# Kernel tuning notes

Hardware: AMD Instinct MI355X
Metric: run time of the kernel (lower is better)

The kernel has to match this reference:

```python
import jax, jax.numpy as jnp
import numpy as np

N = 8192
NFEAT = 512
NHID = 512
NCLASS = 8
EPS = 1e-9
ADJ_P = 0.01  # edge density


def setup_inputs() -> dict:
    key = jax.random.key(0)
    ks = jax.random.split(key, 16)
    adj = (jax.random.uniform(ks[0], (N, N)) < ADJ_P).astype(jnp.float32)
    x = jax.random.normal(ks[1], (N, NFEAT), dtype=jnp.float32)
    s_in = 1.0 / np.sqrt(NFEAT)
    s_h = 1.0 / np.sqrt(NHID)
    return {
        "adj": adj,
        "x": x,
        "gcn1_W": jax.random.normal(ks[2], (NFEAT, NHID), jnp.float32) * s_in,
        "gcn1_b": jnp.zeros((NHID,), jnp.float32),
        "Qw": jax.random.normal(ks[3], (NHID, NHID), jnp.float32) * s_h,
        "Qb": jnp.zeros((NHID,), jnp.float32),
        "Kw": jax.random.normal(ks[4], (NHID, NHID), jnp.float32) * s_h,
        "Kb": jnp.zeros((NHID,), jnp.float32),
        "Vw": jax.random.normal(ks[5], (NHID, NHID), jnp.float32) * s_h,
        "Vb": jnp.zeros((NHID,), jnp.float32),
        "ln_g": jnp.ones((NHID,), jnp.float32),
        "ln_b": jnp.zeros((NHID,), jnp.float32),
        "gcn2_W": jax.random.normal(ks[6], (NHID, NCLASS), jnp.float32) * s_h,
        "gcn2_b": jnp.zeros((NCLASS,), jnp.float32),
    }


def _gcn_norm(a):
    # symmetric degree normalization D^{-1/2} A D^{-1/2}, degrees = row sums
    d_inv_sqrt = jax.lax.rsqrt(a.sum(axis=1) + EPS)  # [N]
    return d_inv_sqrt[:, None] * a * d_inv_sqrt[None, :]


def _layer_norm(x, g, b):
    mu = x.mean(axis=-1, keepdims=True)
    var = x.var(axis=-1, keepdims=True)
    return (x - mu) * jax.lax.rsqrt(var + 1e-5) * g + b


def reference(adj, x, gcn1_W, gcn1_b, Qw, Qb, Kw, Kb, Vw, Vb, ln_g, ln_b, gcn2_W, gcn2_b):
    # GraphConvolution: adj @ (x W) + b, then ReLU
    h = jax.nn.relu(adj @ (x @ gcn1_W) + gcn1_b)  # [N, NHID]
    Qh = h @ Qw + Qb
    Kh = h @ Kw + Kb
    Vh = h @ Vw + Vb
    # adjacency-masked dense scores (multiplicative mask, as in original)
    A_tilde = adj * (Qh @ Kh.T)  # [N, N]
    attention = jax.nn.softmax(A_tilde, axis=1)
    X_tilde = _gcn_norm(attention) @ Vh  # [N, NHID]
    X_tilde = _layer_norm(X_tilde, ln_g, ln_b)
    z = adj @ (X_tilde @ gcn2_W) + gcn2_b  # [N, NCLASS]
    return jax.nn.softmax(z, axis=1)
```

## Files before the change

### kernel.cpp

```cpp
#include <hip/hip_runtime.h>
#include <math.h>

#define N_NODES 8192
#define NFEAT 512
#define NHID 512
#define NCLASS 8
#define RCAP 192
#define KSPLIT 1536

__device__ inline ushort f2bf(float f) {
  uint32_t u = __float_as_uint(f);
  uint32_t r = u + 0x7fffu + ((u >> 16) & 1u);
  return (ushort)(r >> 16);
}
__device__ inline float bf2f(ushort h) { return __uint_as_float(((uint32_t)h) << 16); }

__global__ __launch_bounds__(256) void build_ell(const float* __restrict__ adj,
                                                 int* __restrict__ colidx,
                                                 int* __restrict__ deg) {
  int row = blockIdx.x;
  __shared__ int cnt;
  __shared__ int cols[RCAP];
  if (threadIdx.x == 0) cnt = 0;
  __syncthreads();
  const float4* arow = (const float4*)(adj + (size_t)row * N_NODES);
  for (int i = threadIdx.x; i < N_NODES / 4; i += 256) {
    float4 v = arow[i];
    int base = i * 4;
    if (v.x > 0.5f) { int p = atomicAdd(&cnt, 1); if (p < RCAP) cols[p] = base; }
    if (v.y > 0.5f) { int p = atomicAdd(&cnt, 1); if (p < RCAP) cols[p] = base + 1; }
    if (v.z > 0.5f) { int p = atomicAdd(&cnt, 1); if (p < RCAP) cols[p] = base + 2; }
    if (v.w > 0.5f) { int p = atomicAdd(&cnt, 1); if (p < RCAP) cols[p] = base + 3; }
  }
  __syncthreads();
  int d = cnt < RCAP ? cnt : RCAP;
  if (threadIdx.x == 0) deg[row] = d;
  for (int i = threadIdx.x; i < d; i += 256) colidx[(size_t)row * RCAP + i] = cols[i];
}

__global__ void transpose512(const float* __restrict__ in, float* __restrict__ out) {
  __shared__ float tile[32][33];
  int x = blockIdx.x * 32 + threadIdx.x;
  int y0 = blockIdx.y * 32;
  for (int i = threadIdx.y; i < 32; i += 8)
    tile[i][threadIdx.x] = in[(size_t)(y0 + i) * 512 + x];
  __syncthreads();
  int xo = blockIdx.y * 32 + threadIdx.x;
  int yo0 = blockIdx.x * 32;
  for (int i = threadIdx.y; i < 32; i += 8)
    out[(size_t)(yo0 + i) * 512 + xo] = tile[threadIdx.x][i];
}

__global__ __launch_bounds__(256) void sgemm64x128(const float* __restrict__ A,
                                                   const float* __restrict__ B,
                                                   const float* __restrict__ bias,
                                                   float* __restrict__ C,
                                                   int M, int Nn, int K, int ldc) {
  __shared__ float As[16][68];
  __shared__ float Bs[16][132];
  const int tid = threadIdx.x;
  const int bm = blockIdx.y * 64, bn = blockIdx.x * 128;
  const int tx = tid & 15, ty = tid >> 4;
  const int arow = tid >> 2, acol = (tid & 3) << 2;
  const int brow = tid >> 4, bcol = (tid & 15) << 2;
  float acc[4][8];
#pragma unroll
  for (int i = 0; i < 4; ++i)
#pragma unroll
    for (int j = 0; j < 8; ++j) acc[i][j] = 0.f;
  const float* Ap = A + (size_t)(bm + arow) * K + acol;
  const float* Bp = B + (size_t)brow * Nn + bn + bcol;
  float4 av = *(const float4*)(Ap);
  float4 bv0 = *(const float4*)(Bp);
  float4 bv1 = *(const float4*)(Bp + 64);
  for (int k0 = 0; k0 < K; k0 += 16) {
    if (k0) __syncthreads();
    As[acol + 0][arow] = av.x;
    As[acol + 1][arow] = av.y;
    As[acol + 2][arow] = av.z;
    As[acol + 3][arow] = av.w;
    *(float4*)&Bs[brow][bcol] = bv0;
    *(float4*)&Bs[brow][bcol + 64] = bv1;
    __syncthreads();
    int kn = (k0 + 16 < K) ? k0 + 16 : 0;
    av = *(const float4*)(Ap + kn);
    bv0 = *(const float4*)(Bp + (size_t)kn * Nn);
    bv1 = *(const float4*)(Bp + (size_t)kn * Nn + 64);
#pragma unroll
    for (int kk = 0; kk < 16; ++kk) {
      float4 a = *(const float4*)&As[kk][ty << 2];
      float4 b0 = *(const float4*)&Bs[kk][tx << 2];
      float4 b1 = *(const float4*)&Bs[kk][(tx << 2) + 64];
      float ar[4] = {a.x, a.y, a.z, a.w};
      float br[8] = {b0.x, b0.y, b0.z, b0.w, b1.x, b1.y, b1.z, b1.w};
#pragma unroll
      for (int i = 0; i < 4; ++i)
#pragma unroll
        for (int j = 0; j < 8; ++j) acc[i][j] = fmaf(ar[i], br[j], acc[i][j]);
    }
  }
#pragma unroll
  for (int i = 0; i < 4; ++i) {
    int r = bm + (ty << 2) + i;
    float4 o0 = make_float4(acc[i][0], acc[i][1], acc[i][2], acc[i][3]);
    float4 o1 = make_float4(acc[i][4], acc[i][5], acc[i][6], acc[i][7]);
    if (bias) {
      const float4 z0 = *(const float4*)(bias + bn + (tx << 2));
      const float4 z1 = *(const float4*)(bias + bn + 64 + (tx << 2));
      o0.x += z0.x; o0.y += z0.y; o0.z += z0.z; o0.w += z0.w;
      o1.x += z1.x; o1.y += z1.y; o1.z += z1.z; o1.w += z1.w;
    }
    *(float4*)(C + (size_t)r * ldc + bn + (tx << 2)) = o0;
    *(float4*)(C + (size_t)r * ldc + bn + 64 + (tx << 2)) = o1;
  }
}

__global__ __launch_bounds__(256) void split_a(const float* __restrict__ A, ushort* __restrict__ As) {
  int idx = blockIdx.x * 256 + threadIdx.x;
  int m = idx >> 7, t = idx & 127;
  float4 v = ((const float4*)(A + (size_t)m * 512))[t];
  ushort4 hi, lo;
  hi.x = f2bf(v.x); hi.y = f2bf(v.y); hi.z = f2bf(v.z); hi.w = f2bf(v.w);
  lo.x = f2bf(v.x - bf2f(hi.x)); lo.y = f2bf(v.y - bf2f(hi.y));
  lo.z = f2bf(v.z - bf2f(hi.z)); lo.w = f2bf(v.w - bf2f(hi.w));
  ushort* row = As + (size_t)m * KSPLIT;
  ((ushort4*)row)[t] = hi;
  ((ushort4*)(row + 512))[t] = hi;
  ((ushort4*)(row + 1024))[t] = lo;
}

__global__ __launch_bounds__(256) void split_bt(const float* __restrict__ B, ushort* __restrict__ Bt, int Nn) {
  int idx = blockIdx.x * 256 + threadIdx.x;
  int n = idx / 384, t = idx % 384;
  int sec = t >> 7;
  int k0 = (t & 127) << 2;
  ushort4 o;
  float f0 = B[(size_t)(k0 + 0) * Nn + n];
  float f1 = B[(size_t)(k0 + 1) * Nn + n];
  float f2 = B[(size_t)(k0 + 2) * Nn + n];
  float f3 = B[(size_t)(k0 + 3) * Nn + n];
  if (sec == 1) {
    o.x = f2bf(f0 - bf2f(f2bf(f0))); o.y = f2bf(f1 - bf2f(f2bf(f1)));
    o.z = f2bf(f2 - bf2f(f2bf(f2))); o.w = f2bf(f3 - bf2f(f2bf(f3)));
  } else {
    o.x = f2bf(f0); o.y = f2bf(f1); o.z = f2bf(f2); o.w = f2bf(f3);
  }
  ((ushort4*)(Bt + (size_t)n * KSPLIT))[t] = o;
}

__global__ __launch_bounds__(256) void split_bt_cat(const float* __restrict__ Mm, const float* __restrict__ Vw,
                                                    ushort* __restrict__ Bt) {
  int idx = blockIdx.x * 256 + threadIdx.x;
  int n = idx / 384, t = idx % 384;
  const float* src = (n < 512) ? (Mm + n) : (Vw + (n - 512));
  int sec = t >> 7;
  int k0 = (t & 127) << 2;
  ushort4 o;
  float f0 = src[(size_t)(k0 + 0) * 512];
  float f1 = src[(size_t)(k0 + 1) * 512];
  float f2 = src[(size_t)(k0 + 2) * 512];
  float f3 = src[(size_t)(k0 + 3) * 512];
  if (sec == 1) {
    o.x = f2bf(f0 - bf2f(f2bf(f0))); o.y = f2bf(f1 - bf2f(f2bf(f1)));
    o.z = f2bf(f2 - bf2f(f2bf(f2))); o.w = f2bf(f3 - bf2f(f2bf(f3)));
  } else {
    o.x = f2bf(f0); o.y = f2bf(f1); o.z = f2bf(f2); o.w = f2bf(f3);
  }
  ((ushort4*)(Bt + (size_t)n * KSPLIT))[t] = o;
}

__global__ void build_bcat(const float* __restrict__ Vb, float* __restrict__ bcat) {
  int i = blockIdx.x * 256 + threadIdx.x;
  bcat[i] = (i < 512) ? 0.f : Vb[i - 512];
}

using frag_ab = __attribute__((ext_vector_type(8))) short;
using frag_cd = __attribute__((ext_vector_type(4))) float;

__global__ __launch_bounds__(256) void mfma_gemm_bt(const ushort* __restrict__ A,
                                                    const ushort* __restrict__ Bt,
                                                    const float* __restrict__ bias,
                                                    float* __restrict__ C,
                                                    int M, int N, int K, int ldc) {
  __shared__ __align__(16) ushort Atile[128 * 64];
  __shared__ __align__(16) ushort Btile[128 * 64];
  const int tid = threadIdx.x;
  const int w = tid >> 6, lane = tid & 63;
  const int m0 = blockIdx.y * 128, n0 = blockIdx.x * 128;
  const int wm = (w >> 1) * 64, wn = (w & 1) * 64;
  const int q = lane >> 4, c = lane & 15;

  frag_cd acc[4][4] = {{{0.f, 0.f, 0.f, 0.f}}};
#pragma unroll
  for (int i = 0; i < 4; ++i)
#pragma unroll
    for (int j = 0; j < 4; ++j) acc[i][j] = (frag_cd){0.f, 0.f, 0.f, 0.f};

  const int srow = (w << 3) + (lane >> 3);
  const int scolb = (lane & 7) << 4;
  const uint8_t* gA = (const uint8_t*)A + ((size_t)(m0 + srow) * K) * 2 + scolb;
  const uint8_t* gB = (const uint8_t*)Bt + ((size_t)(n0 + srow) * K) * 2 + scolb;
  const size_t rowpitch = (size_t)K * 2;

  for (int k0 = 0; k0 < K; k0 += 64) {
    const size_t kb = (size_t)k0 * 2;
#pragma unroll
    for (int r = 0; r < 4; ++r) {
      __builtin_amdgcn_global_load_lds(
          (const __attribute__((address_space(1))) uint32_t*)(gA + (size_t)(r * 32) * rowpitch + kb),
          (__attribute__((address_space(3))) uint32_t*)((uint8_t*)Atile + r * 4096 + w * 1024), 16, 0, 0);
      __builtin_amdgcn_global_load_lds(
          (const __attribute__((address_space(1))) uint32_t*)(gB + (size_t)(r * 32) * rowpitch + kb),
          (__attribute__((address_space(3))) uint32_t*)((uint8_t*)Btile + r * 4096 + w * 1024), 16, 0, 0);
    }
    __syncthreads();
#pragma unroll
    for (int kk = 0; kk < 2; ++kk) {
      frag_ab af[4], bf[4];
#pragma unroll
      for (int i = 0; i < 4; ++i) {
        af[i] = *(const frag_ab*)((const uint8_t*)Atile + (wm + i * 16 + c) * 128 + kk * 64 + q * 16);
        bf[i] = *(const frag_ab*)((const uint8_t*)Btile + (wn + i * 16 + c) * 128 + kk * 64 + q * 16);
      }
#pragma unroll
      for (int i = 0; i < 4; ++i)
#pragma unroll
        for (int j = 0; j < 4; ++j)
          acc[i][j] = __builtin_amdgcn_mfma_f32_16x16x32_bf16(af[i], bf[j], acc[i][j], 0, 0, 0);
    }
    __syncthreads();
  }
#pragma unroll
  for (int j = 0; j < 4; ++j) {
    int col = n0 + wn + j * 16 + c;
    float bv = bias ? bias[col] : 0.f;
#pragma unroll
    for (int i = 0; i < 4; ++i) {
      int row = m0 + wm + i * 16 + q * 4;
#pragma unroll
      for (int r = 0; r < 4; ++r)
        C[(size_t)(row + r) * ldc + col] = acc[i][j][r] + bv;
    }
  }
}

__global__ __launch_bounds__(64) void bias_prep(const float* __restrict__ Qw, const float* __restrict__ Kw,
                                                const float* __restrict__ Qb, const float* __restrict__ Kb,
                                                float* __restrict__ u, float* __restrict__ w,
                                                float* __restrict__ cbuf) {
  int k = blockIdx.x;
  int lane = threadIdx.x;
  if (k == NHID) {
    float s = 0.f;
    for (int j = lane; j < NHID; j += 64) s = fmaf(Qb[j], Kb[j], s);
#pragma unroll
    for (int o = 32; o > 0; o >>= 1) s += __shfl_down(s, o, 64);
    if (lane == 0) cbuf[0] = s;
    return;
  }
  float su = 0.f, sw = 0.f;
  for (int j = lane; j < NHID; j += 64) {
    su = fmaf(Qw[(size_t)k * NHID + j], Kb[j], su);
    sw = fmaf(Kw[(size_t)k * NHID + j], Qb[j], sw);
  }
#pragma unroll
  for (int o = 32; o > 0; o >>= 1) { su += __shfl_down(su, o, 64); sw += __shfl_down(sw, o, 64); }
  if (lane == 0) { u[k] = su; w[k] = sw; }
}

__global__ __launch_bounds__(128) void spmm_bias_relu(const float* __restrict__ xW,
                                                      const int* __restrict__ colidx,
                                                      const int* __restrict__ deg,
                                                      const float* __restrict__ bias,
                                                      float* __restrict__ h,
                                                      ushort* __restrict__ Hs) {
  int row = blockIdx.x;
  int d = deg[row];
  __shared__ int scols[RCAP];
  int t = threadIdx.x;
  for (int i = t; i < d; i += 128) scols[i] = colidx[(size_t)row * RCAP + i];
  __syncthreads();
  float4 acc = make_float4(0.f, 0.f, 0.f, 0.f);
  int e = 0;
  for (; e + 8 <= d; e += 8) {
    float4 v0 = ((const float4*)(xW + (size_t)scols[e + 0] * NHID))[t];
    float4 v1 = ((const float4*)(xW + (size_t)scols[e + 1] * NHID))[t];
    float4 v2 = ((const float4*)(xW + (size_t)scols[e + 2] * NHID))[t];
    float4 v3 = ((const float4*)(xW + (size_t)scols[e + 3] * NHID))[t];
    float4 v4 = ((const float4*)(xW + (size_t)scols[e + 4] * NHID))[t];
    float4 v5 = ((const float4*)(xW + (size_t)scols[e + 5] * NHID))[t];
    float4 v6 = ((const float4*)(xW + (size_t)scols[e + 6] * NHID))[t];
    float4 v7 = ((const float4*)(xW + (size_t)scols[e + 7] * NHID))[t];
    acc.x += ((v0.x + v1.x) + (v2.x + v3.x)) + ((v4.x + v5.x) + (v6.x + v7.x));
    acc.y += ((v0.y + v1.y) + (v2.y + v3.y)) + ((v4.y + v5.y) + (v6.y + v7.y));
    acc.z += ((v0.z + v1.z) + (v2.z + v3.z)) + ((v4.z + v5.z) + (v6.z + v7.z));
    acc.w += ((v0.w + v1.w) + (v2.w + v3.w)) + ((v4.w + v5.w) + (v6.w + v7.w));
  }
  for (; e < d; ++e) {
    float4 v = ((const float4*)(xW + (size_t)scols[e] * NHID))[t];
    acc.x += v.x; acc.y += v.y; acc.z += v.z; acc.w += v.w;
  }
  float4 bv = ((const float4*)bias)[t];
  float4 o = make_float4(fmaxf(acc.x + bv.x, 0.f), fmaxf(acc.y + bv.y, 0.f),
                         fmaxf(acc.z + bv.z, 0.f), fmaxf(acc.w + bv.w, 0.f));
  ((float4*)(h + (size_t)row * NHID))[t] = o;
  ushort4 hi, lo;
  hi.x = f2bf(o.x); hi.y = f2bf(o.y); hi.z = f2bf(o.z); hi.w = f2bf(o.w);
  lo.x = f2bf(o.x - bf2f(hi.x)); lo.y = f2bf(o.y - bf2f(hi.y));
  lo.z = f2bf(o.z - bf2f(hi.z)); lo.w = f2bf(o.w - bf2f(hi.w));
  ushort* hr = Hs + (size_t)row * KSPLIT;
  ((ushort4*)hr)[t] = hi;
  ((ushort4*)(hr + 512))[t] = hi;
  ((ushort4*)(hr + 1024))[t] = lo;
}

__global__ __launch_bounds__(256) void dual_matvec(const float* __restrict__ h, const float* __restrict__ u,
                                                   const float* __restrict__ w, float* __restrict__ a_vec,
                                                   float* __restrict__ b_vec) {
  int t = threadIdx.x;
  int wv = t >> 6, lane = t & 63;
  int row = blockIdx.x * 4 + wv;
  const float2* hr = (const float2*)(h + (size_t)row * NHID);
  const float2* ur = (const float2*)u;
  const float2* wr = (const float2*)w;
  float sa = 0.f, sb = 0.f;
  for (int i = lane; i < NHID / 2; i += 64) {
    float2 hv = hr[i], uv = ur[i], wv2 = wr[i];
    sa = fmaf(hv.x, uv.x, sa); sa = fmaf(hv.y, uv.y, sa);
    sb = fmaf(hv.x, wv2.x, sb); sb = fmaf(hv.y, wv2.y, sb);
  }
#pragma unroll
  for (int o = 32; o > 0; o >>= 1) { sa += __shfl_down(sa, o, 64); sb += __shfl_down(sb, o, 64); }
  if (lane == 0) { a_vec[row] = sa; b_vec[row] = sb; }
}

__global__ void zero_vec(float* __restrict__ T) { T[threadIdx.x] = 0.f; }

__global__ __launch_bounds__(256) void colsum_atomic(const float* __restrict__ Vh, int ldv,
                                                     float* __restrict__ T) {
  int t = threadIdx.x;
  int r0 = blockIdx.x * 128;
  float2 s = make_float2(0.f, 0.f);
  for (int r = 0; r < 128; ++r) {
    float2 v = ((const float2*)(Vh + (size_t)(r0 + r) * ldv))[t];
    s.x += v.x;
    s.y += v.y;
  }
  atomicAdd(&T[2 * t], s.x);
  atomicAdd(&T[2 * t + 1], s.y);
}

__global__ __launch_bounds__(256) void edge_softmax_agg(const float* __restrict__ G, int ldg,
                                                        const float* __restrict__ h,
                                                        const float* __restrict__ Vh, int ldv,
                                                        const int* __restrict__ colidx, const int* __restrict__ deg,
                                                        const float* __restrict__ a_vec, const float* __restrict__ b_vec,
                                                        const float* __restrict__ cbuf, const float* __restrict__ T,
                                                        const float* __restrict__ lng, const float* __restrict__ lnb,
                                                        float* __restrict__ Xt) {
  __shared__ float gs[4][NHID];
  __shared__ int scols[4][RCAP];
  __shared__ float sbv[4][RCAP];
  __shared__ float sv[4][RCAP];
  int t = threadIdx.x, wv = t >> 6, lane = t & 63;
  int row = blockIdx.x * 4 + wv;
  int d = deg[row];
  const float4* gr = (const float4*)(G + (size_t)row * ldg);
  ((float4*)gs[wv])[lane] = gr[lane];
  ((float4*)gs[wv])[64 + lane] = gr[64 + lane];
  for (int i = lane; i < d; i += 64) {
    int cc = colidx[(size_t)row * RCAP + i];
    scols[wv][i] = cc;
    sbv[wv][i] = b_vec[cc];
  }
  __syncthreads();
  float ai = a_vec[row] + cbuf[0];
  int q = lane >> 4, u = lane & 15;
  const float4* gq = (const float4*)gs[wv] + u;
  for (int e0 = 0; e0 < d; e0 += 4) {
    int e = e0 + q;
    bool act = e < d;
    int col = act ? scols[wv][e] : 0;
    const float4* hr = (const float4*)(h + (size_t)col * NHID) + u;
    float s_a = 0.f, s_b = 0.f;
#pragma unroll
    for (int it = 0; it < 8; it += 2) {
      float4 h0 = hr[it * 16], g0 = gq[it * 16];
      float4 h1 = hr[(it + 1) * 16], g1 = gq[(it + 1) * 16];
      s_a = fmaf(h0.x, g0.x, s_a); s_a = fmaf(h0.y, g0.y, s_a);
      s_a = fmaf(h0.z, g0.z, s_a); s_a = fmaf(h0.w, g0.w, s_a);
      s_b = fmaf(h1.x, g1.x, s_b); s_b = fmaf(h1.y, g1.y, s_b);
      s_b = fmaf(h1.z, g1.z, s_b); s_b = fmaf(h1.w, g1.w, s_b);
    }
    float s = s_a + s_b;
    s += __shfl_down(s, 8, 16);
    s += __shfl_down(s, 4, 16);
    s += __shfl_down(s, 2, 16);
    s += __shfl_down(s, 1, 16);
    if (u == 0 && act) sv[wv][e] = s + ai + sbv[wv][e];
  }
  __syncthreads();
  float m = 0.f;
  for (int i = lane; i < d; i += 64) m = fmaxf(m, sv[wv][i]);
#pragma unroll
  for (int o = 32; o > 0; o >>= 1) m = fmaxf(m, __shfl_xor(m, o, 64));
  float ssum = 0.f;
  for (int i = lane; i < d; i += 64) {
    float ex = expf(sv[wv][i] - m);
    sv[wv][i] = ex;
    ssum += ex;
  }
#pragma unroll
  for (int o = 32; o > 0; o >>= 1) ssum += __shfl_xor(ssum, o, 64);
  float em = expf(-m);
  float inv = 1.f / (ssum + (float)(N_NODES - d) * em);
  float ci = em * inv;
  __syncthreads();
  float4 a0 = make_float4(0.f, 0.f, 0.f, 0.f), a1 = a0;
  for (int e = 0; e < d; ++e) {
    float we = sv[wv][e] * inv;
    if (we > 1e-12f) {
      const float4* vr = (const float4*)(Vh + (size_t)scols[wv][e] * ldv);
      float4 v0 = vr[lane * 2], v1 = vr[lane * 2 + 1];
      a0.x = fmaf(we, v0.x, a0.x); a0.y = fmaf(we, v0.y, a0.y);
      a0.z = fmaf(we, v0.z, a0.z); a0.w = fmaf(we, v0.w, a0.w);
      a1.x = fmaf(we, v1.x, a1.x); a1.y = fmaf(we, v1.y, a1.y);
      a1.z = fmaf(we, v1.z, a1.z); a1.w = fmaf(we, v1.w, a1.w);
    }
  }
  float4 t0 = ((const float4*)T)[lane * 2], t1 = ((const float4*)T)[lane * 2 + 1];
  a0.x = fmaf(ci, t0.x, a0.x); a0.y = fmaf(ci, t0.y, a0.y);
  a0.z = fmaf(ci, t0.z, a0.z); a0.w = fmaf(ci, t0.w, a0.w);
  a1.x = fmaf(ci, t1.x, a1.x); a1.y = fmaf(ci, t1.y, a1.y);
  a1.z = fmaf(ci, t1.z, a1.z); a1.w = fmaf(ci, t1.w, a1.w);
  float s1 = ((a0.x + a0.y) + (a0.z + a0.w)) + ((a1.x + a1.y) + (a1.z + a1.w));
  float s2 = ((a0.x * a0.x + a0.y * a0.y) + (a0.z * a0.z + a0.w * a0.w)) +
             ((a1.x * a1.x + a1.y * a1.y) + (a1.z * a1.z + a1.w * a1.w));
#pragma unroll
  for (int o = 32; o > 0; o >>= 1) { s1 += __shfl_xor(s1, o, 64); s2 += __shfl_xor(s2, o, 64); }
  float mu = s1 * (1.f / NHID);
  float var = s2 * (1.f / NHID) - mu * mu;
  float rstd = rsqrtf(var + 1e-5f);
  float4 g0 = ((const float4*)lng)[lane * 2], g1 = ((const float4*)lng)[lane * 2 + 1];
  float4 b0 = ((const float4*)lnb)[lane * 2], b1 = ((const float4*)lnb)[lane * 2 + 1];
  float4 o0, o1;
  o0.x = (a0.x - mu) * rstd * g0.x + b0.x;
  o0.y = (a0.y - mu) * rstd * g0.y + b0.y;
  o0.z = (a0.z - mu) * rstd * g0.z + b0.z;
  o0.w = (a0.w - mu) * rstd * g0.w + b0.w;
  o1.x = (a1.x - mu) * rstd * g1.x + b1.x;
  o1.y = (a1.y - mu) * rstd * g1.y + b1.y;
  o1.z = (a1.z - mu) * rstd * g1.z + b1.z;
  o1.w = (a1.w - mu) * rstd * g1.w + b1.w;
  float4* xr = (float4*)(Xt + (size_t)row * NHID);
  xr[lane * 2] = o0;
  xr[lane * 2 + 1] = o1;
}

__global__ __launch_bounds__(256) void xt_w2(const float* __restrict__ Xt, const float* __restrict__ W2,
                                             float* __restrict__ Y) {
  __shared__ float w2s[NHID * NCLASS];
  int t = threadIdx.x;
  for (int i = t; i < NHID * NCLASS; i += 256) w2s[i] = W2[i];
  __syncthreads();
  int wv = t >> 6, lane = t & 63;
  int row = blockIdx.x * 4 + wv;
  const float4* xr = (const float4*)(Xt + (size_t)row * NHID);
  float4 x0 = xr[lane * 2], x1 = xr[lane * 2 + 1];
  float xv[8] = {x0.x, x0.y, x0.z, x0.w, x1.x, x1.y, x1.z, x1.w};
  float acc[NCLASS];
#pragma unroll
  for (int c = 0; c < NCLASS; ++c) acc[c] = 0.f;
#pragma unroll
  for (int kk = 0; kk < 8; ++kk) {
    int k = lane * 8 + kk;
#pragma unroll
    for (int c = 0; c < NCLASS; ++c) acc[c] = fmaf(xv[kk], w2s[k * NCLASS + c], acc[c]);
  }
#pragma unroll
  for (int c = 0; c < NCLASS; ++c)
#pragma unroll
    for (int o = 32; o > 0; o >>= 1) acc[c] += __shfl_down(acc[c], o, 64);
  if (lane == 0) {
    *(float4*)(Y + (size_t)row * NCLASS) = make_float4(acc[0], acc[1], acc[2], acc[3]);
    *(float4*)(Y + (size_t)row * NCLASS + 4) = make_float4(acc[4], acc[5], acc[6], acc[7]);
  }
}

__global__ __launch_bounds__(256) void final_spmm_softmax(const float* __restrict__ Y,
                                                          const int* __restrict__ colidx,
                                                          const int* __restrict__ deg,
                                                          const float* __restrict__ b2,
                                                          float* __restrict__ out) {
  int t = threadIdx.x;
  int wv = t >> 6, lane = t & 63;
  int row = blockIdx.x * 4 + wv;
  int d = deg[row];
  const int* cols = colidx + (size_t)row * RCAP;
  float acc[8];
#pragma unroll
  for (int c = 0; c < 8; ++c) acc[c] = 0.f;
  for (int e = lane; e < d; e += 64) {
    int col = cols[e];
    const float4* yr = (const float4*)(Y + (size_t)col * 8);
    float4 y0 = yr[0], y1 = yr[1];
    acc[0] += y0.x; acc[1] += y0.y; acc[2] += y0.z; acc[3] += y0.w;
    acc[4] += y1.x; acc[5] += y1.y; acc[6] += y1.z; acc[7] += y1.w;
  }
#pragma unroll
  for (int c = 0; c < 8; ++c)
#pragma unroll
    for (int o = 32; o > 0; o >>= 1) acc[c] += __shfl_down(acc[c], o, 64);
  if (lane == 0) {
    float z[8];
    float m = -1e30f;
#pragma unroll
    for (int c = 0; c < 8; ++c) { z[c] = acc[c] + b2[c]; m = fmaxf(m, z[c]); }
    float s = 0.f;
#pragma unroll
    for (int c = 0; c < 8; ++c) { z[c] = expf(z[c] - m); s += z[c]; }
    float inv = 1.f / s;
    *(float4*)(out + (size_t)row * 8) = make_float4(z[0] * inv, z[1] * inv, z[2] * inv, z[3] * inv);
    *(float4*)(out + (size_t)row * 8 + 4) = make_float4(z[4] * inv, z[5] * inv, z[6] * inv, z[7] * inv);
  }
}

extern "C" void kernel_launch(void* const* d_in, const int* in_sizes, int n_in,
                              void* d_out, int out_size, void* d_ws, size_t ws_size,
                              hipStream_t stream) {
  const float* adj = (const float*)d_in[0];
  const float* x = (const float*)d_in[1];
  const float* W1 = (const float*)d_in[2];
  const float* b1 = (const float*)d_in[3];
  const float* Qw = (const float*)d_in[4];
  const float* Qb = (const float*)d_in[5];
  const float* Kw = (const float*)d_in[6];
  const float* Kb = (const float*)d_in[7];
  const float* Vw = (const float*)d_in[8];
  const float* Vb = (const float*)d_in[9];
  const float* ln_g = (const float*)d_in[10];
  const float* ln_b = (const float*)d_in[11];
  const float* W2 = (const float*)d_in[12];
  const float* b2 = (const float*)d_in[13];
  float* out = (float*)d_out;

  char* ws = (char*)d_ws;
  size_t off = 0;
  auto alloc = [&](size_t bytes) -> void* {
    void* p = ws + off;
    off = (off + bytes + 255) & ~(size_t)255;
    return p;
  };
  int* colidx = (int*)alloc((size_t)N_NODES * RCAP * 4);
  int* deg = (int*)alloc((size_t)N_NODES * 4);
  float* bufA = (float*)alloc((size_t)N_NODES * NHID * 4);
  float* bufB = (float*)alloc((size_t)N_NODES * NHID * 4);
  float* GVh = (float*)alloc((size_t)N_NODES * 1024 * 4);
  ushort* Xs = (ushort*)alloc((size_t)N_NODES * KSPLIT * 2);
  ushort* Hs = (ushort*)alloc((size_t)N_NODES * KSPLIT * 2);
  ushort* W1ts = (ushort*)alloc((size_t)512 * KSPLIT * 2);
  ushort* Bcts = (ushort*)alloc((size_t)1024 * KSPLIT * 2);
  float* KwT = (float*)alloc((size_t)512 * 512 * 4);
  float* Mmat = (float*)alloc((size_t)512 * 512 * 4);
  float* bcat = (float*)alloc((size_t)1024 * 4);
  float* a_vec = (float*)alloc((size_t)N_NODES * 4);
  float* b_vec = (float*)alloc((size_t)N_NODES * 4);
  float* u_vec = (float*)alloc((size_t)NHID * 4);
  float* w_vec = (float*)alloc((size_t)NHID * 4);
  float* cbuf = (float*)alloc(256);
  float* T = (float*)alloc((size_t)NHID * 4);
  float* Y = (float*)alloc((size_t)N_NODES * NCLASS * 4);
  (void)in_sizes; (void)n_in; (void)out_size; (void)ws_size;

  build_ell<<<N_NODES, 256, 0, stream>>>(adj, colidx, deg);
  transpose512<<<dim3(16, 16), dim3(32, 8), 0, stream>>>(Kw, KwT);
  bias_prep<<<NHID + 1, 64, 0, stream>>>(Qw, Kw, Qb, Kb, u_vec, w_vec, cbuf);
  sgemm64x128<<<dim3(4, 8), 256, 0, stream>>>(Qw, KwT, nullptr, Mmat, 512, 512, 512, 512);
  split_a<<<(N_NODES * 128) / 256, 256, 0, stream>>>(x, Xs);
  split_bt<<<(512 * 384) / 256, 256, 0, stream>>>(W1, W1ts, 512);
  mfma_gemm_bt<<<dim3(4, 64), 256, 0, stream>>>(Xs, W1ts, nullptr, bufA, N_NODES, 512, KSPLIT, 512);
  spmm_bias_relu<<<N_NODES, 128, 0, stream>>>(bufA, colidx, deg, b1, bufB, Hs);
  split_bt_cat<<<(1024 * 384) / 256, 256, 0, stream>>>(Mmat, Vw, Bcts);
  build_bcat<<<4, 256, 0, stream>>>(Vb, bcat);
  mfma_gemm_bt<<<dim3(8, 64), 256, 0, stream>>>(Hs, Bcts, bcat, GVh, N_NODES, 1024, KSPLIT, 1024);
  dual_matvec<<<N_NODES / 4, 256, 0, stream>>>(bufB, u_vec, w_vec, a_vec, b_vec);
  zero_vec<<<1, 512, 0, stream>>>(T);
  colsum_atomic<<<64, 256, 0, stream>>>(GVh + 512, 1024, T);
  edge_softmax_agg<<<N_NODES / 4, 256, 0, stream>>>(GVh, 1024, bufB, GVh + 512, 1024, colidx, deg,
                                                    a_vec, b_vec, cbuf, T, ln_g, ln_b, bufA);
  xt_w2<<<N_NODES / 4, 256, 0, stream>>>(bufA, W2, Y);
  final_spmm_softmax<<<N_NODES / 4, 256, 0, stream>>>(Y, colidx, deg, b2, out);
}
```

Measured before the change: 850.7 us.

## Slice sparse gathers by column range and shrink split-bf16 A operand

The SpMM and the edge-score gathers are split into 8 passes, each touching only neighbour columns inside one 1024-row window. The aim is to keep each window of the gathered matrix resident in cache. The split-bf16 A operand drops its duplicated hi copy: the MFMA GEMM now reuses the first 512 columns for two of the three K-segments, which cuts A-side memory and write traffic. The bias/ReLU/bf16 split and the dual matvec are fused into one finalize kernel, and scores are staged through a global edge buffer before a separate softmax/aggregate/layernorm kernel. The cost is many more launches, repeated colidx scans, and a read-modify-write of h on every slice.

After: 812.3 us. -4.5%, faster.

```diff
diff --git a/kernel.cpp b/kernel.cpp
--- a/kernel.cpp
+++ b/kernel.cpp
@@ -6,7 +6,9 @@
 #define NHID 512
 #define NCLASS 8
 #define RCAP 192
-#define KSPLIT 1536
+#define KB_SPLIT 1536
+#define KA_SPLIT 1024
+#define NSLICE 8
 
 __device__ inline ushort f2bf(float f) {
   uint32_t u = __float_as_uint(f);
@@ -53,7 +55,6 @@
 
 __global__ __launch_bounds__(256) void sgemm64x128(const float* __restrict__ A,
                                                    const float* __restrict__ B,
-                                                   const float* __restrict__ bias,
                                                    float* __restrict__ C,
                                                    int M, int Nn, int K, int ldc) {
   __shared__ float As[16][68];
@@ -102,20 +103,14 @@
 #pragma unroll
   for (int i = 0; i < 4; ++i) {
     int r = bm + (ty << 2) + i;
-    float4 o0 = make_float4(acc[i][0], acc[i][1], acc[i][2], acc[i][3]);
-    float4 o1 = make_float4(acc[i][4], acc[i][5], acc[i][6], acc[i][7]);
-    if (bias) {
-      const float4 z0 = *(const float4*)(bias + bn + (tx << 2));
-      const float4 z1 = *(const float4*)(bias + bn + 64 + (tx << 2));
-      o0.x += z0.x; o0.y += z0.y; o0.z += z0.z; o0.w += z0.w;
-      o1.x += z1.x; o1.y += z1.y; o1.z += z1.z; o1.w += z1.w;
-    }
-    *(float4*)(C + (size_t)r * ldc + bn + (tx << 2)) = o0;
-    *(float4*)(C + (size_t)r * ldc + bn + 64 + (tx << 2)) = o1;
-  }
-}
-
-__global__ __launch_bounds__(256) void split_a(const float* __restrict__ A, ushort* __restrict__ As) {
+    *(float4*)(C + (size_t)r * ldc + bn + (tx << 2)) =
+        make_float4(acc[i][0], acc[i][1], acc[i][2], acc[i][3]);
+    *(float4*)(C + (size_t)r * ldc + bn + 64 + (tx << 2)) =
+        make_float4(acc[i][4], acc[i][5], acc[i][6], acc[i][7]);
+  }
+}
+
+__global__ __launch_bounds__(256) void split_a2(const float* __restrict__ A, ushort* __restrict__ As) {
   int idx = blockIdx.x * 256 + threadIdx.x;
   int m = idx >> 7, t = idx & 127;
   float4 v = ((const float4*)(A + (size_t)m * 512))[t];
@@ -123,10 +118,9 @@
   hi.x = f2bf(v.x); hi.y = f2bf(v.y); hi.z = f2bf(v.z); hi.w = f2bf(v.w);
   lo.x = f2bf(v.x - bf2f(hi.x)); lo.y = f2bf(v.y - bf2f(hi.y));
   lo.z = f2bf(v.z - bf2f(hi.z)); lo.w = f2bf(v.w - bf2f(hi.w));
-  ushort* row = As + (size_t)m * KSPLIT;
+  ushort* row = As + (size_t)m * KA_SPLIT;
   ((ushort4*)row)[t] = hi;
-  ((ushort4*)(row + 512))[t] = hi;
-  ((ushort4*)(row + 1024))[t] = lo;
+  ((ushort4*)(row + 512))[t] = lo;
 }
 
 __global__ __launch_bounds__(256) void split_bt(const float* __restrict__ B, ushort* __restrict__ Bt, int Nn) {
@@ -145,7 +139,7 @@
   } else {
     o.x = f2bf(f0); o.y = f2bf(f1); o.z = f2bf(f2); o.w = f2bf(f3);
   }
-  ((ushort4*)(Bt + (size_t)n * KSPLIT))[t] = o;
+  ((ushort4*)(Bt + (size_t)n * KB_SPLIT))[t] = o;
 }
 
 __global__ __launch_bounds__(256) void split_bt_cat(const float* __restrict__ Mm, const float* __restrict__ Vw,
@@ -166,7 +160,7 @@
   } else {
     o.x = f2bf(f0); o.y = f2bf(f1); o.z = f2bf(f2); o.w = f2bf(f3);
   }
-  ((ushort4*)(Bt + (size_t)n * KSPLIT))[t] = o;
+  ((ushort4*)(Bt + (size_t)n * KB_SPLIT))[t] = o;
 }
 
 __global__ void build_bcat(const float* __restrict__ Vb, float* __restrict__ bcat) {
@@ -181,16 +175,16 @@
                                                     const ushort* __restrict__ Bt,
                                                     const float* __restrict__ bias,
                                                     float* __restrict__ C,
-                                                    int M, int N, int K, int ldc) {
+                                                    int ldc) {
   __shared__ __align__(16) ushort Atile[128 * 64];
   __shared__ __align__(16) ushort Btile[128 * 64];
   const int tid = threadIdx.x;
   const int w = tid >> 6, lane = tid & 63;
   const int m0 = blockIdx.y * 128, n0 = blockIdx.x * 128;
   const int wm = (w >> 1) * 64, wn = (w & 1) * 64;
-  const int q = lane >> 4, c = lane & 15;
-
-  frag_cd acc[4][4] = {{{0.f, 0.f, 0.f, 0.f}}};
+  const int q = lane >> 4, c16 = lane & 15;
+
+  frag_cd acc[4][4];
 #pragma unroll
   for (int i = 0; i < 4; ++i)
 #pragma unroll
@@ -198,19 +192,19 @@
 
   const int srow = (w << 3) + (lane >> 3);
   const int scolb = (lane & 7) << 4;
-  const uint8_t* gA = (const uint8_t*)A + ((size_t)(m0 + srow) * K) * 2 + scolb;
-  const uint8_t* gB = (const uint8_t*)Bt + ((size_t)(n0 + srow) * K) * 2 + scolb;
-  const size_t rowpitch = (size_t)K * 2;
-
-  for (int k0 = 0; k0 < K; k0 += 64) {
-    const size_t kb = (size_t)k0 * 2;
+  const uint8_t* gA = (const uint8_t*)A + (size_t)(m0 + srow) * (KA_SPLIT * 2) + scolb;
+  const uint8_t* gB = (const uint8_t*)Bt + (size_t)(n0 + srow) * (KB_SPLIT * 2) + scolb;
+
+  for (int c = 0; c < 24; ++c) {
+    const size_t kaB = (size_t)((c < 8 ? c : c - 8) * 128);
+    const size_t kbB = (size_t)(c * 128);
 #pragma unroll
     for (int r = 0; r < 4; ++r) {
       __builtin_amdgcn_global_load_lds(
-          (const __attribute__((address_space(1))) uint32_t*)(gA + (size_t)(r * 32) * rowpitch + kb),
+          (const __attribute__((address_space(1))) uint32_t*)(gA + (size_t)(r * 32) * (KA_SPLIT * 2) + kaB),
           (__attribute__((address_space(3))) uint32_t*)((uint8_t*)Atile + r * 4096 + w * 1024), 16, 0, 0);
       __builtin_amdgcn_global_load_lds(
-          (const __attribute__((address_space(1))) uint32_t*)(gB + (size_t)(r * 32) * rowpitch + kb),
+          (const __attribute__((address_space(1))) uint32_t*)(gB + (size_t)(r * 32) * (KB_SPLIT * 2) + kbB),
           (__attribute__((address_space(3))) uint32_t*)((uint8_t*)Btile + r * 4096 + w * 1024), 16, 0, 0);
     }
     __syncthreads();
@@ -219,8 +213,8 @@
       frag_ab af[4], bf[4];
 #pragma unroll
       for (int i = 0; i < 4; ++i) {
-        af[i] = *(const frag_ab*)((const uint8_t*)Atile + (wm + i * 16 + c) * 128 + kk * 64 + q * 16);
-        bf[i] = *(const frag_ab*)((const uint8_t*)Btile + (wn + i * 16 + c) * 128 + kk * 64 + q * 16);
+        af[i] = *(const frag_ab*)((const uint8_t*)Atile + (wm + i * 16 + c16) * 128 + kk * 64 + q * 16);
+        bf[i] = *(const frag_ab*)((const uint8_t*)Btile + (wn + i * 16 + c16) * 128 + kk * 64 + q * 16);
       }
 #pragma unroll
       for (int i = 0; i < 4; ++i)
@@ -232,7 +226,7 @@
   }
 #pragma unroll
   for (int j = 0; j < 4; ++j) {
-    int col = n0 + wn + j * 16 + c;
+    int col = n0 + wn + j * 16 + c16;
     float bv = bias ? bias[col] : 0.f;
 #pragma unroll
     for (int i = 0; i < 4; ++i) {
@@ -268,119 +262,102 @@
   if (lane == 0) { u[k] = su; w[k] = sw; }
 }
 
-__global__ __launch_bounds__(128) void spmm_bias_relu(const float* __restrict__ xW,
-                                                      const int* __restrict__ colidx,
-                                                      const int* __restrict__ deg,
-                                                      const float* __restrict__ bias,
-                                                      float* __restrict__ h,
-                                                      ushort* __restrict__ Hs) {
+__global__ __launch_bounds__(128) void spmm_slice(const float* __restrict__ xW,
+                                                  const int* __restrict__ colidx,
+                                                  const int* __restrict__ deg,
+                                                  float* __restrict__ h, int s0, int init) {
   int row = blockIdx.x;
   int d = deg[row];
   __shared__ int scols[RCAP];
+  __shared__ int scnt;
   int t = threadIdx.x;
-  for (int i = t; i < d; i += 128) scols[i] = colidx[(size_t)row * RCAP + i];
-  __syncthreads();
-  float4 acc = make_float4(0.f, 0.f, 0.f, 0.f);
+  if (t == 0) scnt = 0;
+  __syncthreads();
+  int klo = s0 << 10, khi = klo + 1024;
+  for (int i = t; i < d; i += 128) {
+    int c = colidx[(size_t)row * RCAP + i];
+    if (c >= klo && c < khi) { int p = atomicAdd(&scnt, 1); scols[p] = c; }
+  }
+  __syncthreads();
+  int n = scnt;
+  float4 acc = init ? make_float4(0.f, 0.f, 0.f, 0.f) : ((float4*)(h + (size_t)row * NHID))[t];
   int e = 0;
-  for (; e + 8 <= d; e += 8) {
+  for (; e + 4 <= n; e += 4) {
     float4 v0 = ((const float4*)(xW + (size_t)scols[e + 0] * NHID))[t];
     float4 v1 = ((const float4*)(xW + (size_t)scols[e + 1] * NHID))[t];
     float4 v2 = ((const float4*)(xW + (size_t)scols[e + 2] * NHID))[t];
     float4 v3 = ((const float4*)(xW + (size_t)scols[e + 3] * NHID))[t];
-    float4 v4 = ((const float4*)(xW + (size_t)scols[e + 4] * NHID))[t];
-    float4 v5 = ((const float4*)(xW + (size_t)scols[e + 5] * NHID))[t];
-    float4 v6 = ((const float4*)(xW + (size_t)scols[e + 6] * NHID))[t];
-    float4 v7 = ((const float4*)(xW + (size_t)scols[e + 7] * NHID))[t];
-    acc.x += ((v0.x + v1.x) + (v2.x + v3.x)) + ((v4.x + v5.x) + (v6.x + v7.x));
-    acc.y += ((v0.y + v1.y) + (v2.y + v3.y)) + ((v4.y + v5.y) + (v6.y + v7.y));
-    acc.z += ((v0.z + v1.z) + (v2.z + v3.z)) + ((v4.z + v5.z) + (v6.z + v7.z));
-    acc.w += ((v0.w + v1.w) + (v2.w + v3.w)) + ((v4.w + v5.w) + (v6.w + v7.w));
-  }
-  for (; e < d; ++e) {
+    acc.x += (v0.x + v1.x) + (v2.x + v3.x);
+    acc.y += (v0.y + v1.y) + (v2.y + v3.y);
+    acc.z += (v0.z + v1.z) + (v2.z + v3.z);
+    acc.w += (v0.w + v1.w) + (v2.w + v3.w);
+  }
+  for (; e < n; ++e) {
     float4 v = ((const float4*)(xW + (size_t)scols[e] * NHID))[t];
     acc.x += v.x; acc.y += v.y; acc.z += v.z; acc.w += v.w;
   }
-  float4 bv = ((const float4*)bias)[t];
-  float4 o = make_float4(fmaxf(acc.x + bv.x, 0.f), fmaxf(acc.y + bv.y, 0.f),
-                         fmaxf(acc.z + bv.z, 0.f), fmaxf(acc.w + bv.w, 0.f));
+  ((float4*)(h + (size_t)row * NHID))[t] = acc;
+}
+
+__global__ __launch_bounds__(128) void h_finalize(float* __restrict__ h, const float* __restrict__ b1,
+                                                  const float* __restrict__ u, const float* __restrict__ w,
+                                                  ushort* __restrict__ Hs, float* __restrict__ a_vec,
+                                                  float* __restrict__ b_vec) {
+  __shared__ float ra[2], rb[2];
+  int row = blockIdx.x, t = threadIdx.x;
+  int wv = t >> 6, lane = t & 63;
+  float4 v = ((float4*)(h + (size_t)row * NHID))[t];
+  float4 bv = ((const float4*)b1)[t];
+  float4 o = make_float4(fmaxf(v.x + bv.x, 0.f), fmaxf(v.y + bv.y, 0.f),
+                         fmaxf(v.z + bv.z, 0.f), fmaxf(v.w + bv.w, 0.f));
   ((float4*)(h + (size_t)row * NHID))[t] = o;
   ushort4 hi, lo;
   hi.x = f2bf(o.x); hi.y = f2bf(o.y); hi.z = f2bf(o.z); hi.w = f2bf(o.w);
   lo.x = f2bf(o.x - bf2f(hi.x)); lo.y = f2bf(o.y - bf2f(hi.y));
   lo.z = f2bf(o.z - bf2f(hi.z)); lo.w = f2bf(o.w - bf2f(hi.w));
-  ushort* hr = Hs + (size_t)row * KSPLIT;
+  ushort* hr = Hs + (size_t)row * KA_SPLIT;
   ((ushort4*)hr)[t] = hi;
-  ((ushort4*)(hr + 512))[t] = hi;
-  ((ushort4*)(hr + 1024))[t] = lo;
-}
-
-__global__ __launch_bounds__(256) void dual_matvec(const float* __restrict__ h, const float* __restrict__ u,
-                                                   const float* __restrict__ w, float* __restrict__ a_vec,
-                                                   float* __restrict__ b_vec) {
-  int t = threadIdx.x;
-  int wv = t >> 6, lane = t & 63;
-  int row = blockIdx.x * 4 + wv;
-  const float2* hr = (const float2*)(h + (size_t)row * NHID);
-  const float2* ur = (const float2*)u;
-  const float2* wr = (const float2*)w;
-  float sa = 0.f, sb = 0.f;
-  for (int i = lane; i < NHID / 2; i += 64) {
-    float2 hv = hr[i], uv = ur[i], wv2 = wr[i];
-    sa = fmaf(hv.x, uv.x, sa); sa = fmaf(hv.y, uv.y, sa);
-    sb = fmaf(hv.x, wv2.x, sb); sb = fmaf(hv.y, wv2.y, sb);
-  }
-#pragma unroll
-  for (int o = 32; o > 0; o >>= 1) { sa += __shfl_down(sa, o, 64); sb += __shfl_down(sb, o, 64); }
-  if (lane == 0) { a_vec[row] = sa; b_vec[row] = sb; }
-}
-
-__global__ void zero_vec(float* __restrict__ T) { T[threadIdx.x] = 0.f; }
-
-__global__ __launch_bounds__(256) void colsum_atomic(const float* __restrict__ Vh, int ldv,
-                                                     float* __restrict__ T) {
-  int t = threadIdx.x;
-  int r0 = blockIdx.x * 128;
-  float2 s = make_float2(0.f, 0.f);
-  for (int r = 0; r < 128; ++r) {
-    float2 v = ((const float2*)(Vh + (size_t)(r0 + r) * ldv))[t];
-    s.x += v.x;
-    s.y += v.y;
-  }
-  atomicAdd(&T[2 * t], s.x);
-  atomicAdd(&T[2 * t + 1], s.y);
-}
-
-__global__ __launch_bounds__(256) void edge_softmax_agg(const float* __restrict__ G, int ldg,
-                                                        const float* __restrict__ h,
-                                                        const float* __restrict__ Vh, int ldv,
-                                                        const int* __restrict__ colidx, const int* __restrict__ deg,
-                                                        const float* __restrict__ a_vec, const float* __restrict__ b_vec,
-                                                        const float* __restrict__ cbuf, const float* __restrict__ T,
-                                                        const float* __restrict__ lng, const float* __restrict__ lnb,
-                                                        float* __restrict__ Xt) {
+  ((ushort4*)(hr + 512))[t] = lo;
+  float4 uv = ((const float4*)u)[t], wv4 = ((const float4*)w)[t];
+  float sa = fmaf(o.x, uv.x, fmaf(o.y, uv.y, fmaf(o.z, uv.z, o.w * uv.w)));
+  float sb = fmaf(o.x, wv4.x, fmaf(o.y, wv4.y, fmaf(o.z, wv4.z, o.w * wv4.w)));
+#pragma unroll
+  for (int off = 32; off > 0; off >>= 1) { sa += __shfl_down(sa, off, 64); sb += __shfl_down(sb, off, 64); }
+  if (lane == 0) { ra[wv] = sa; rb[wv] = sb; }
+  __syncthreads();
+  if (t == 0) { a_vec[row] = ra[0] + ra[1]; b_vec[row] = rb[0] + rb[1]; }
+}
+
+__global__ __launch_bounds__(256) void score_slice(const float* __restrict__ G, int ldg,
+                                                   const float* __restrict__ h,
+                                                   const int* __restrict__ colidx,
+                                                   const int* __restrict__ deg, int s0,
+                                                   float* __restrict__ score) {
   __shared__ float gs[4][NHID];
-  __shared__ int scols[4][RCAP];
-  __shared__ float sbv[4][RCAP];
-  __shared__ float sv[4][RCAP];
+  __shared__ int sel_e[4][RCAP];
+  __shared__ int sel_c[4][RCAP];
+  __shared__ int cnt[4];
   int t = threadIdx.x, wv = t >> 6, lane = t & 63;
   int row = blockIdx.x * 4 + wv;
   int d = deg[row];
+  if (lane == 0) cnt[wv] = 0;
+  __syncthreads();
+  int klo = s0 << 10, khi = klo + 1024;
+  for (int i = lane; i < d; i += 64) {
+    int c = colidx[(size_t)row * RCAP + i];
+    if (c >= klo && c < khi) { int p = atomicAdd(&cnt[wv], 1); sel_e[wv][p] = i; sel_c[wv][p] = c; }
+  }
   const float4* gr = (const float4*)(G + (size_t)row * ldg);
   ((float4*)gs[wv])[lane] = gr[lane];
   ((float4*)gs[wv])[64 + lane] = gr[64 + lane];
-  for (int i = lane; i < d; i += 64) {
-    int cc = colidx[(size_t)row * RCAP + i];
-    scols[wv][i] = cc;
-    sbv[wv][i] = b_vec[cc];
-  }
-  __syncthreads();
-  float ai = a_vec[row] + cbuf[0];
+  __syncthreads();
+  int n = cnt[wv];
   int q = lane >> 4, u = lane & 15;
   const float4* gq = (const float4*)gs[wv] + u;
-  for (int e0 = 0; e0 < d; e0 += 4) {
-    int e = e0 + q;
-    bool act = e < d;
-    int col = act ? scols[wv][e] : 0;
+  for (int e0 = 0; e0 < n; e0 += 4) {
+    int idx = e0 + q;
+    bool act = idx < n;
+    int col = sel_c[wv][act ? idx : 0];
     const float4* hr = (const float4*)(h + (size_t)col * NHID) + u;
     float s_a = 0.f, s_b = 0.f;
 #pragma unroll
@@ -397,7 +374,44 @@
     s += __shfl_down(s, 4, 16);
     s += __shfl_down(s, 2, 16);
     s += __shfl_down(s, 1, 16);
-    if (u == 0 && act) sv[wv][e] = s + ai + sbv[wv][e];
+    if (u == 0 && act) score[(size_t)row * RCAP + sel_e[wv][idx]] = s;
+  }
+}
+
+__global__ void zero_vec(float* __restrict__ T) { T[threadIdx.x] = 0.f; }
+
+__global__ __launch_bounds__(256) void colsum_atomic(const float* __restrict__ Vh, int ldv,
+                                                     float* __restrict__ T) {
+  int t = threadIdx.x;
+  int r0 = blockIdx.x * 128;
+  float2 s = make_float2(0.f, 0.f);
+  for (int r = 0; r < 128; ++r) {
+    float2 v = ((const float2*)(Vh + (size_t)(r0 + r) * ldv))[t];
+    s.x += v.x;
+    s.y += v.y;
+  }
+  atomicAdd(&T[2 * t], s.x);
+  atomicAdd(&T[2 * t + 1], s.y);
+}
+
+__global__ __launch_bounds__(256) void softmax_agg_ln(const float* __restrict__ score,
+                                                      const int* __restrict__ colidx, const int* __restrict__ deg,
+                                                      const float* __restrict__ a_vec, const float* __restrict__ b_vec,
+                                                      const float* __restrict__ cbuf,
+                                                      const float* __restrict__ Vh, int ldv,
+                                                      const float* __restrict__ T,
+                                                      const float* __restrict__ lng, const float* __restrict__ lnb,
+                                                      float* __restrict__ Xt) {
+  __shared__ int scols[4][RCAP];
+  __shared__ float sv[4][RCAP];
+  int t = threadIdx.x, wv = t >> 6, lane = t & 63;
+  int row = blockIdx.x * 4 + wv;
+  int d = deg[row];
+  float ai = a_vec[row] + cbuf[0];
+  for (int i = lane; i < d; i += 64) {
+    int c = colidx[(size_t)row * RCAP + i];
+    scols[wv][i] = c;
+    sv[wv][i] = score[(size_t)row * RCAP + i] + ai + b_vec[c];
   }
   __syncthreads();
   float m = 0.f;
@@ -556,13 +570,14 @@
   float* bufA = (float*)alloc((size_t)N_NODES * NHID * 4);
   float* bufB = (float*)alloc((size_t)N_NODES * NHID * 4);
   float* GVh = (float*)alloc((size_t)N_NODES * 1024 * 4);
-  ushort* Xs = (ushort*)alloc((size_t)N_NODES * KSPLIT * 2);
-  ushort* Hs = (ushort*)alloc((size_t)N_NODES * KSPLIT * 2);
-  ushort* W1ts = (ushort*)alloc((size_t)512 * KSPLIT * 2);
-  ushort* Bcts = (ushort*)alloc((size_t)1024 * KSPLIT * 2);
+  ushort* Xs = (ushort*)alloc((size_t)N_NODES * KA_SPLIT * 2);
+  ushort* Hs = (ushort*)alloc((size_t)N_NODES * KA_SPLIT * 2);
+  ushort* W1ts = (ushort*)alloc((size_t)512 * KB_SPLIT * 2);
+  ushort* Bcts = (ushort*)alloc((size_t)1024 * KB_SPLIT * 2);
   float* KwT = (float*)alloc((size_t)512 * 512 * 4);
   float* Mmat = (float*)alloc((size_t)512 * 512 * 4);
   float* bcat = (float*)alloc((size_t)1024 * 4);
+  float* edge_s = (float*)alloc((size_t)N_NODES * RCAP * 4);
   float* a_vec = (float*)alloc((size_t)N_NODES * 4);
   float* b_vec = (float*)alloc((size_t)N_NODES * 4);
   float* u_vec = (float*)alloc((size_t)NHID * 4);
@@ -575,19 +590,22 @@
   build_ell<<<N_NODES, 256, 0, stream>>>(adj, colidx, deg);
   transpose512<<<dim3(16, 16), dim3(32, 8), 0, stream>>>(Kw, KwT);
   bias_prep<<<NHID + 1, 64, 0, stream>>>(Qw, Kw, Qb, Kb, u_vec, w_vec, cbuf);
-  sgemm64x128<<<dim3(4, 8), 256, 0, stream>>>(Qw, KwT, nullptr, Mmat, 512, 512, 512, 512);
-  split_a<<<(N_NODES * 128) / 256, 256, 0, stream>>>(x, Xs);
+  sgemm64x128<<<dim3(4, 8), 256, 0, stream>>>(Qw, KwT, Mmat, 512, 512, 512, 512);
+  split_a2<<<(N_NODES * 128) / 256, 256, 0, stream>>>(x, Xs);
   split_bt<<<(512 * 384) / 256, 256, 0, stream>>>(W1, W1ts, 512);
-  mfma_gemm_bt<<<dim3(4, 64), 256, 0, stream>>>(Xs, W1ts, nullptr, bufA, N_NODES, 512, KSPLIT, 512);
-  spmm_bias_relu<<<N_NODES, 128, 0, stream>>>(bufA, colidx, deg, b1, bufB, Hs);
+  mfma_gemm_bt<<<dim3(4, 64), 256, 0, stream>>>(Xs, W1ts, nullptr, bufA, 512);
+  for (int s = 0; s < NSLICE; ++s)
+    spmm_slice<<<N_NODES, 128, 0, stream>>>(bufA, colidx, deg, bufB, s, s == 0);
+  h_finalize<<<N_NODES, 128, 0, stream>>>(bufB, b1, u_vec, w_vec, Hs, a_vec, b_vec);
   split_bt_cat<<<(1024 * 384) / 256, 256, 0, stream>>>(Mmat, Vw, Bcts);
   build_bcat<<<4, 256, 0, stream>>>(Vb, bcat);
-  mfma_gemm_bt<<<dim3(8, 64), 256, 0, stream>>>(Hs, Bcts, bcat, GVh, N_NODES, 1024, KSPLIT, 1024);
-  dual_matvec<<<N_NODES / 4, 256, 0, stream>>>(bufB, u_vec, w_vec, a_vec, b_vec);
+  mfma_gemm_bt<<<dim3(8, 64), 256, 0, stream>>>(Hs, Bcts, bcat, GVh, 1024);
   zero_vec<<<1, 512, 0, stream>>>(T);
   colsum_atomic<<<64, 256, 0, stream>>>(GVh + 512, 1024, T);
-  edge_softmax_agg<<<N_NODES / 4, 256, 0, stream>>>(GVh, 1024, bufB, GVh + 512, 1024, colidx, deg,
-                                                    a_vec, b_vec, cbuf, T, ln_g, ln_b, bufA);
+  for (int s = 0; s < NSLICE; ++s)
+    score_slice<<<N_NODES / 4, 256, 0, stream>>>(GVh, 1024, bufB, colidx, deg, s, edge_s);
+  softmax_agg_ln<<<N_NODES / 4, 256, 0, stream>>>(edge_s, colidx, deg, a_vec, b_vec, cbuf,
+                                                  GVh + 512, 1024, T, ln_g, ln_b, bufA);
   xt_w2<<<N_NODES / 4, 256, 0, stream>>>(bufA, W2, Y);
   final_spmm_softmax<<<N_NODES / 4, 256, 0, stream>>>(Y, colidx, deg, b2, out);
 }
```
